# Kernel tuning notes

Hardware: AMD Instinct MI355X
Metric: run time of the kernel (lower is better)

The kernel has to match this reference:

```python
import jax, jax.numpy as jnp
import numpy as np

DIM = 256


def setup_inputs() -> dict:
    key = jax.random.key(0)
    ks = jax.random.split(key, 10)
    d = DIM
    inp = {
        "agent": jax.random.normal(ks[0], (64, d), dtype=jnp.float32),
        "x": jax.random.normal(ks[1], (8, 4096, d), dtype=jnp.float32),
        # parameters (stored as [in, out]; y = x @ W + b)
        "W_qkv": jax.random.normal(ks[2], (d, 3 * d), dtype=jnp.float32) * (d ** -0.5),
        "b_qkv": jnp.zeros((3 * d,), dtype=jnp.float32),
        "W_agent": jax.random.normal(ks[3], (d, 2 * d), dtype=jnp.float32) * (d ** -0.5),
        "b_agent": jnp.zeros((2 * d,), dtype=jnp.float32),
        "W_fc1": jax.random.normal(ks[4], (d, d), dtype=jnp.float32) * (d ** -0.5),
        "b_fc1": jnp.zeros((d,), dtype=jnp.float32),
        "W_fc2": jax.random.normal(ks[5], (d, d), dtype=jnp.float32) * (d ** -0.5),
        "b_fc2": jnp.zeros((d,), dtype=jnp.float32),
    }
    return inp


def reference(agent, x, W_qkv, b_qkv, W_agent, b_agent, W_fc1, b_fc1, W_fc2, b_fc2):
    d = x.shape[-1]
    scale = d ** -0.5
    # qkv projection of tokens: [B,N,3d] -> q,k,v each [B,N,d]
    qkv = x @ W_qkv + b_qkv
    q, k, v = jnp.split(qkv, 3, axis=-1)
    # agent projection: [K,2d] -> q_agent,k_agent each [K,d]
    ag = agent @ W_agent + b_agent
    q_agent, k_agent = jnp.split(ag, 2, axis=-1)
    # stage 1: agents attend over tokens -> [B,K,N]
    attn1 = jax.nn.softmax(jnp.einsum('kd,bnd->bkn', q_agent, k) * scale, axis=-1)
    va = jnp.einsum('bkn,bnd->bkd', attn1, v)  # [B,K,d]
    va = va @ W_fc1 + b_fc1
    # stage 2: tokens attend over agents -> [B,N,K]
    attn2 = jax.nn.softmax(jnp.einsum('bnd,kd->bnk', q, k_agent) * scale, axis=-1)
    out = jnp.einsum('bnk,bkd->bnd', attn2, va)  # [B,N,d]
    out = out @ W_fc2 + b_fc2
    return out + x
```

## Files before the change

### kernel.cpp

```cpp
#include <hip/hip_runtime.h>
#include <stdint.h>
#include <string.h>

#define BB 8
#define NN 4096
#define DD 256
#define SCALE 0.0625f
#define XS2 264

using frag_ab = __attribute__((ext_vector_type(8))) short;
using frag_cd = __attribute__((ext_vector_type(4))) float;

__device__ __forceinline__ unsigned short f2bf(float f) {
    union { float f; unsigned u; } a; a.f = f;
    unsigned r = a.u + 0x7FFFu + ((a.u >> 16) & 1u);
    return (unsigned short)(r >> 16);
}
__device__ __forceinline__ float bf2f(unsigned short h) {
    union { unsigned u; float f; } a; a.u = ((unsigned)h) << 16;
    return a.f;
}

__global__ __launch_bounds__(256) void k_setup(
    const float* __restrict__ agent, const float* __restrict__ Wag,
    const float* __restrict__ bag, const float* __restrict__ Wqkv,
    const float* __restrict__ bqkv, const float* __restrict__ Wfc1,
    const float* __restrict__ bfc1, const float* __restrict__ Wfc2,
    unsigned short* __restrict__ P12t, float* __restrict__ c2,
    unsigned short* __restrict__ W3b, float* __restrict__ b3)
{
    __shared__ float arow[256];
    __shared__ float red[256];
    const int bx = blockIdx.x, tid = threadIdx.x;
    if (bx < 128) {
        const int c = bx;
        const int woff = (c < 64) ? 256 : 0;
        const int aoff = (c < 64) ? 0 : 256;
        const int row = c & 63;
        float s = bag[aoff + tid];
        for (int o = 0; o < 256; ++o) s += agent[row * 256 + o] * Wag[o * 512 + aoff + tid];
        arow[tid] = s;
        __syncthreads();
        float p = 0.f;
        for (int o = 0; o < 256; ++o) p += Wqkv[tid * 768 + woff + o] * arow[o];
        P12t[(size_t)c * 256 + tid] = f2bf(SCALE * p);
        if (c >= 64) {
            red[tid] = bqkv[woff + tid] * arow[tid];
            __syncthreads();
            for (int st = 128; st; st >>= 1) {
                if (tid < st) red[tid] += red[tid + st];
                __syncthreads();
            }
            if (tid == 0) c2[c - 64] = SCALE * red[0];
        }
    } else if (bx < 384) {
        const int i = bx - 128;
        float t = 0.f;
        for (int o = 0; o < 256; ++o) t += Wqkv[i * 768 + 512 + o] * Wfc1[o * 256 + tid];
        arow[tid] = t;
        __syncthreads();
        float p = 0.f;
        for (int k = 0; k < 256; ++k) p += arow[k] * Wfc2[k * 256 + tid];
        W3b[(size_t)i * 256 + tid] = f2bf(p);
    } else {
        float t = bfc1[tid];
        for (int o = 0; o < 256; ++o) t += bqkv[512 + o] * Wfc1[o * 256 + tid];
        arow[tid] = t;
        __syncthreads();
        float p = 0.f;
        for (int k = 0; k < 256; ++k) p += arow[k] * Wfc2[k * 256 + tid];
        b3[tid] = p;
    }
}

__global__ __launch_bounds__(256) void k_xlogits(
    const float* __restrict__ x, const unsigned short* __restrict__ P12t,
    const float* __restrict__ c2, unsigned short* __restrict__ xt,
    unsigned short* __restrict__ p1, unsigned short* __restrict__ p2b,
    float* __restrict__ statS)
{
    __shared__ unsigned short xtile[32 * XS2];
    __shared__ unsigned short Bs[128 * 72];
    __shared__ float Ss[2][64];
    const int chunk = blockIdx.x, b = blockIdx.y;
    const int n0 = chunk * 32;
    const int tid = threadIdx.x;
    const int w = tid >> 6, lane = tid & 63;
    const int ml = lane & 15, q = lane >> 4;
    const int rt = w & 1, cg = w >> 1;

#pragma unroll
    for (int p = 0; p < 8; ++p) {
        int idx = p * 256 + tid;
        int tok = idx >> 6, d = (idx & 63) * 4;
        float4 v = *(const float4*)&x[(size_t)(b * 4096 + n0 + tok) * 256 + d];
        unsigned short u[4] = {f2bf(v.x), f2bf(v.y), f2bf(v.z), f2bf(v.w)};
        uint2 pk; memcpy(&pk, u, 8);
        *(uint2*)&xtile[tok * XS2 + d] = pk;
    }
    __syncthreads();
#pragma unroll
    for (int p = 0; p < 8; ++p) {
        int idx = p * 256 + tid;
        int d = idx >> 3, seg = idx & 7;
        unsigned short u[4];
#pragma unroll
        for (int k = 0; k < 4; ++k) u[k] = xtile[(seg * 4 + k) * XS2 + d];
        uint2 pk; memcpy(&pk, u, 8);
        *(uint2*)&xt[(size_t)(b * 256 + d) * 4096 + n0 + seg * 4] = pk;
    }

    frag_cd acc[4];
#pragma unroll
    for (int j = 0; j < 4; ++j)
#pragma unroll
        for (int r = 0; r < 4; ++r) acc[j][r] = 0.f;

    for (int kb = 0; kb < 256; kb += 64) {
        __syncthreads();
#pragma unroll
        for (int p = 0; p < 4; ++p) {
            int idx = p * 256 + tid;
            int r = idx >> 3, c = (idx & 7) * 8;
            *(uint4*)&Bs[r * 72 + c] = *(const uint4*)&P12t[(size_t)r * 256 + kb + c];
        }
        __syncthreads();
#pragma unroll
        for (int ks = 0; ks < 2; ++ks) {
            const int kk = ks * 32 + q * 8;
            frag_ab a = *(const frag_ab*)&xtile[(rt * 16 + ml) * XS2 + kb + kk];
#pragma unroll
            for (int j = 0; j < 4; ++j) {
                frag_ab bf = *(const frag_ab*)&Bs[(cg * 64 + j * 16 + ml) * 72 + kk];
                acc[j] = __builtin_amdgcn_mfma_f32_16x16x32_bf16(a, bf, acc[j], 0, 0, 0);
            }
        }
    }

    if (cg == 0) {
#pragma unroll
        for (int j = 0; j < 4; ++j) {
            const int ag = j * 16 + ml;
            float e[4];
#pragma unroll
            for (int r = 0; r < 4; ++r) e[r] = __expf(acc[j][r]);
            unsigned short u[4] = {f2bf(e[0]), f2bf(e[1]), f2bf(e[2]), f2bf(e[3])};
            uint2 pk; memcpy(&pk, u, 8);
            *(uint2*)&p1[(size_t)(b * 64 + ag) * 4096 + n0 + rt * 16 + q * 4] = pk;
            float s = e[0] + e[1] + e[2] + e[3];
            s += __shfl_xor(s, 16);
            s += __shfl_xor(s, 32);
            if (q == 0) Ss[rt][ag] = s;
        }
    } else {
        float cc[4];
#pragma unroll
        for (int j = 0; j < 4; ++j) cc[j] = c2[j * 16 + ml];
#pragma unroll
        for (int r = 0; r < 4; ++r) {
            float e[4], s = 0.f;
#pragma unroll
            for (int j = 0; j < 4; ++j) {
                e[j] = __expf(acc[j][r] + cc[j]);
                s += e[j];
            }
#pragma unroll
            for (int mask = 1; mask <= 8; mask <<= 1) s += __shfl_xor(s, mask);
            float inv = 1.f / s;
            const int tok = n0 + rt * 16 + q * 4 + r;
#pragma unroll
            for (int j = 0; j < 4; ++j)
                p2b[(size_t)(b * 4096 + tok) * 64 + j * 16 + ml] = f2bf(e[j] * inv);
        }
    }
    __syncthreads();
    if (tid < 64)
        statS[(size_t)(b * 64 + tid) * 128 + chunk] = Ss[0][tid] + Ss[1][tid];
}

__global__ __launch_bounds__(256) void k_va(
    const unsigned short* __restrict__ p1, const float* __restrict__ statS,
    const unsigned short* __restrict__ xt, unsigned short* __restrict__ part)
{
    __shared__ unsigned short As[64 * 152];
    __shared__ unsigned short Bs[64 * 152];
    __shared__ float Rs[4][64], Inv[64];
    const int s = blockIdx.x, dh = blockIdx.y, b = blockIdx.z;
    const int tid = threadIdx.x;
    const int w = tid >> 6, lane = tid & 63;
    const int ml = lane & 15, q = lane >> 4;

#pragma unroll
    for (int p = 0; p < 4; ++p) {
        int idx = p * 256 + tid;
        int r = idx >> 4, c = (idx & 15) * 8;
        *(uint4*)&Bs[r * 152 + c] =
            *(const uint4*)&xt[(size_t)(b * 256 + dh * 64 + r) * 4096 + s * 128 + c];
    }
    {
        const int a = tid & 63, qq = tid >> 6;
        const float* ps = &statS[(size_t)(b * 64 + a) * 128 + qq * 32];
        float sum = 0.f;
#pragma unroll
        for (int p = 0; p < 8; ++p) {
            float4 s4 = *(const float4*)&ps[p * 4];
            sum += s4.x + s4.y + s4.z + s4.w;
        }
        Rs[qq][a] = sum;
    }
    __syncthreads();
    if (tid < 64)
        Inv[tid] = 1.f / (Rs[0][tid] + Rs[1][tid] + Rs[2][tid] + Rs[3][tid]);
    __syncthreads();
#pragma unroll
    for (int p = 0; p < 8; ++p) {
        int idx4 = (p * 256 + tid) * 4;
        int ag = idx4 >> 7, t = idx4 & 127;
        uint2 pk = *(const uint2*)&p1[(size_t)(b * 64 + ag) * 4096 + s * 128 + t];
        unsigned short in[4]; memcpy(in, &pk, 8);
        float inv = Inv[ag];
        unsigned short u[4] = {f2bf(bf2f(in[0]) * inv), f2bf(bf2f(in[1]) * inv),
                               f2bf(bf2f(in[2]) * inv), f2bf(bf2f(in[3]) * inv)};
        uint2 po; memcpy(&po, u, 8);
        *(uint2*)&As[ag * 152 + t] = po;
    }
    __syncthreads();

    frag_cd acc[4];
#pragma unroll
    for (int i = 0; i < 4; ++i)
#pragma unroll
        for (int r = 0; r < 4; ++r) acc[i][r] = 0.f;
#pragma unroll
    for (int ks = 0; ks < 4; ++ks) {
        const int kk = ks * 32 + q * 8;
        frag_ab bf = *(const frag_ab*)&Bs[(w * 16 + ml) * 152 + kk];
#pragma unroll
        for (int i = 0; i < 4; ++i) {
            frag_ab a = *(const frag_ab*)&As[(i * 16 + ml) * 152 + kk];
            acc[i] = __builtin_amdgcn_mfma_f32_16x16x32_bf16(a, bf, acc[i], 0, 0, 0);
        }
    }
    const int d = dh * 64 + w * 16 + ml;
#pragma unroll
    for (int i = 0; i < 4; ++i)
#pragma unroll
        for (int r = 0; r < 4; ++r)
            part[(size_t)((s * 8 + b) * 64 + i * 16 + q * 4 + r) * 256 + d] =
                f2bf(acc[i][r]);
}

__global__ __launch_bounds__(256) void k_fc(
    const unsigned short* __restrict__ part, const unsigned short* __restrict__ W3b,
    const float* __restrict__ b3, unsigned short* __restrict__ va3t)
{
    __shared__ float rowb[256];
    const int row = blockIdx.x, tid = threadIdx.x;
    const int b = row >> 6, agc = row & 63;
    float sv = 0.f;
    for (int s = 0; s < 32; ++s)
        sv += bf2f(part[(size_t)((s * 8 + b) * 64 + agc) * 256 + tid]);
    rowb[tid] = sv;
    __syncthreads();
    float s2 = b3[tid];
    for (int k = 0; k < 256; ++k) s2 += rowb[k] * bf2f(W3b[(size_t)k * 256 + tid]);
    va3t[(size_t)(b * 256 + tid) * 64 + agc] = f2bf(s2);
}

__global__ __launch_bounds__(256) void k_stage2(
    const unsigned short* __restrict__ p2b, const unsigned short* __restrict__ va3t,
    const float* __restrict__ x, const float* __restrict__ bfc2,
    float* __restrict__ out)
{
    __shared__ unsigned short Vs[256 * 72];
    __shared__ unsigned short Ps[64 * 72];
    const int n0 = blockIdx.x * 64, b = blockIdx.y;
    const int tid = threadIdx.x;
    const int w = tid >> 6, lane = tid & 63;
    const int ml = lane & 15, q = lane >> 4;

#pragma unroll
    for (int p = 0; p < 8; ++p) {
        int idx = p * 256 + tid;
        int r = idx >> 3, c = (idx & 7) * 8;
        *(uint4*)&Vs[r * 72 + c] = *(const uint4*)&va3t[(size_t)(b * 256 + r) * 64 + c];
    }
#pragma unroll
    for (int p = 0; p < 2; ++p) {
        int idx = p * 256 + tid;
        int r = idx >> 3, c = (idx & 7) * 8;
        *(uint4*)&Ps[r * 72 + c] = *(const uint4*)&p2b[(size_t)(b * 4096 + n0 + r) * 64 + c];
    }
    __syncthreads();

    frag_cd acc[4][4];
#pragma unroll
    for (int i = 0; i < 4; ++i)
#pragma unroll
        for (int j = 0; j < 4; ++j)
#pragma unroll
            for (int r = 0; r < 4; ++r) acc[i][j][r] = 0.f;
#pragma unroll
    for (int ks = 0; ks < 2; ++ks) {
        const int kk = ks * 32 + q * 8;
        frag_ab a[4], bf[4];
#pragma unroll
        for (int i = 0; i < 4; ++i)
            a[i] = *(const frag_ab*)&Vs[(w * 64 + i * 16 + ml) * 72 + kk];
#pragma unroll
        for (int j = 0; j < 4; ++j)
            bf[j] = *(const frag_ab*)&Ps[(j * 16 + ml) * 72 + kk];
#pragma unroll
        for (int i = 0; i < 4; ++i)
#pragma unroll
            for (int j = 0; j < 4; ++j)
                acc[i][j] = __builtin_amdgcn_mfma_f32_16x16x32_bf16(
                    a[i], bf[j], acc[i][j], 0, 0, 0);
    }

#pragma unroll
    for (int i = 0; i < 4; ++i) {
        const int d0 = w * 64 + i * 16 + q * 4;
        float4 bias = *(const float4*)&bfc2[d0];
#pragma unroll
        for (int j = 0; j < 4; ++j) {
            const int tok = n0 + j * 16 + ml;
            size_t ad = (size_t)(b * 4096 + tok) * 256 + d0;
            float4 xr = *(const float4*)&x[ad];
            float4 o;
            o.x = acc[i][j][0] + bias.x + xr.x;
            o.y = acc[i][j][1] + bias.y + xr.y;
            o.z = acc[i][j][2] + bias.z + xr.z;
            o.w = acc[i][j][3] + bias.w + xr.w;
            *(float4*)&out[ad] = o;
        }
    }
}

extern "C" void kernel_launch(void* const* d_in, const int* in_sizes, int n_in,
                              void* d_out, int out_size, void* d_ws, size_t ws_size,
                              hipStream_t stream) {
    const float* agent = (const float*)d_in[0];
    const float* x     = (const float*)d_in[1];
    const float* Wqkv  = (const float*)d_in[2];
    const float* bqkv  = (const float*)d_in[3];
    const float* Wag   = (const float*)d_in[4];
    const float* bag   = (const float*)d_in[5];
    const float* Wfc1  = (const float*)d_in[6];
    const float* bfc1  = (const float*)d_in[7];
    const float* Wfc2  = (const float*)d_in[8];
    const float* bfc2  = (const float*)d_in[9];
    float* out = (float*)d_out;

    char* w = (char*)d_ws;
    size_t off = 0;
    unsigned short* xt   = (unsigned short*)(w + off); off += (size_t)BB * DD * NN * 2;
    unsigned short* p1   = (unsigned short*)(w + off); off += (size_t)BB * 64 * NN * 2;
    unsigned short* p2b  = (unsigned short*)(w + off); off += (size_t)BB * NN * 64 * 2;
    unsigned short* part = (unsigned short*)(w + off); off += (size_t)32 * BB * 64 * 256 * 2;
    float* statS = (float*)(w + off); off += (size_t)BB * 64 * 128 * 4;
    unsigned short* P12t = (unsigned short*)(w + off); off += (size_t)128 * 256 * 2;
    float* c2   = (float*)(w + off); off += 256 * 4;
    unsigned short* W3b = (unsigned short*)(w + off); off += (size_t)256 * 256 * 2;
    float* b3   = (float*)(w + off); off += 256 * 4;
    unsigned short* va3t = (unsigned short*)(w + off); off += (size_t)BB * DD * 64 * 2;

    k_setup<<<385, 256, 0, stream>>>(agent, Wag, bag, Wqkv, bqkv, Wfc1, bfc1, Wfc2,
                                     P12t, c2, W3b, b3);
    k_xlogits<<<dim3(128, BB), 256, 0, stream>>>(x, P12t, c2, xt, p1, p2b, statS);
    k_va<<<dim3(32, 4, BB), 256, 0, stream>>>(p1, statS, xt, part);
    k_fc<<<512, 256, 0, stream>>>(part, W3b, b3, va3t);
    k_stage2<<<dim3(64, BB), 256, 0, stream>>>(p2b, va3t, x, bfc2, out);
}
```

Baseline: 169.7 us.

## Fuse logits and value-aggregation kernels, keeping x tile in shared memory

Merges the logits kernel and the agent-value aggregation kernel into one kernel per 64-token chunk. The bf16 x tile stays in LDS and is reused as the B operand for the P1·x MFMA, so the transposed x copy and the unnormalized p1 matrix no longer go through global memory. Softmax normalization for stage 1 moves into k_fc, which now sums per-chunk statistics and divides after reducing partials. In exchange there are twice as many partial slabs to reduce in k_fc, more registers per thread, strided LDS reads when building the x fragments, and only 512 blocks for the fused kernel.

```diff
diff --git a/kernel.cpp b/kernel.cpp
--- a/kernel.cpp
+++ b/kernel.cpp
@@ -6,7 +6,8 @@
 #define NN 4096
 #define DD 256
 #define SCALE 0.0625f
-#define XS2 264
+#define XS 264
+#define XT 72
 
 using frag_ab = __attribute__((ext_vector_type(8))) short;
 using frag_cd = __attribute__((ext_vector_type(4))) float;
@@ -73,48 +74,37 @@
     }
 }
 
-__global__ __launch_bounds__(256) void k_xlogits(
+__global__ __launch_bounds__(256) void k_fuse(
     const float* __restrict__ x, const unsigned short* __restrict__ P12t,
-    const float* __restrict__ c2, unsigned short* __restrict__ xt,
-    unsigned short* __restrict__ p1, unsigned short* __restrict__ p2b,
-    float* __restrict__ statS)
+    const float* __restrict__ c2, unsigned short* __restrict__ p2b,
+    unsigned short* __restrict__ part, float* __restrict__ statS)
 {
-    __shared__ unsigned short xtile[32 * XS2];
-    __shared__ unsigned short Bs[128 * 72];
-    __shared__ float Ss[2][64];
-    const int chunk = blockIdx.x, b = blockIdx.y;
-    const int n0 = chunk * 32;
+    __shared__ unsigned short xtile[64 * XS];
+    __shared__ unsigned short Bs[128 * XT];
+    __shared__ unsigned short Pl[64 * XT];
+    __shared__ float Ss[4][64];
+    const int s = blockIdx.x, b = blockIdx.y;
+    const int n0 = s * 64;
     const int tid = threadIdx.x;
     const int w = tid >> 6, lane = tid & 63;
     const int ml = lane & 15, q = lane >> 4;
-    const int rt = w & 1, cg = w >> 1;
-
-#pragma unroll
-    for (int p = 0; p < 8; ++p) {
+
+#pragma unroll
+    for (int p = 0; p < 16; ++p) {
         int idx = p * 256 + tid;
         int tok = idx >> 6, d = (idx & 63) * 4;
         float4 v = *(const float4*)&x[(size_t)(b * 4096 + n0 + tok) * 256 + d];
         unsigned short u[4] = {f2bf(v.x), f2bf(v.y), f2bf(v.z), f2bf(v.w)};
         uint2 pk; memcpy(&pk, u, 8);
-        *(uint2*)&xtile[tok * XS2 + d] = pk;
-    }
-    __syncthreads();
-#pragma unroll
-    for (int p = 0; p < 8; ++p) {
-        int idx = p * 256 + tid;
-        int d = idx >> 3, seg = idx & 7;
-        unsigned short u[4];
-#pragma unroll
-        for (int k = 0; k < 4; ++k) u[k] = xtile[(seg * 4 + k) * XS2 + d];
-        uint2 pk; memcpy(&pk, u, 8);
-        *(uint2*)&xt[(size_t)(b * 256 + d) * 4096 + n0 + seg * 4] = pk;
-    }
-
-    frag_cd acc[4];
-#pragma unroll
-    for (int j = 0; j < 4; ++j)
-#pragma unroll
-        for (int r = 0; r < 4; ++r) acc[j][r] = 0.f;
+        *(uint2*)&xtile[tok * XS + d] = pk;
+    }
+    __syncthreads();
+
+    frag_cd acc1[8];
+#pragma unroll
+    for (int j = 0; j < 8; ++j)
+#pragma unroll
+        for (int r = 0; r < 4; ++r) acc1[j][r] = 0.f;
 
     for (int kb = 0; kb < 256; kb += 64) {
         __syncthreads();
@@ -122,145 +112,122 @@
         for (int p = 0; p < 4; ++p) {
             int idx = p * 256 + tid;
             int r = idx >> 3, c = (idx & 7) * 8;
-            *(uint4*)&Bs[r * 72 + c] = *(const uint4*)&P12t[(size_t)r * 256 + kb + c];
+            *(uint4*)&Bs[r * XT + c] = *(const uint4*)&P12t[(size_t)r * 256 + kb + c];
         }
         __syncthreads();
 #pragma unroll
         for (int ks = 0; ks < 2; ++ks) {
             const int kk = ks * 32 + q * 8;
-            frag_ab a = *(const frag_ab*)&xtile[(rt * 16 + ml) * XS2 + kb + kk];
+            frag_ab a = *(const frag_ab*)&xtile[(w * 16 + ml) * XS + kb + kk];
+#pragma unroll
+            for (int j = 0; j < 8; ++j) {
+                frag_ab bf = *(const frag_ab*)&Bs[(j * 16 + ml) * XT + kk];
+                acc1[j] = __builtin_amdgcn_mfma_f32_16x16x32_bf16(a, bf, acc1[j], 0, 0, 0);
+            }
+        }
+    }
+
+    {
+        float cc[4];
+#pragma unroll
+        for (int j = 0; j < 4; ++j) cc[j] = c2[j * 16 + ml];
+#pragma unroll
+        for (int r = 0; r < 4; ++r) {
+            float e[4], sum = 0.f;
 #pragma unroll
             for (int j = 0; j < 4; ++j) {
-                frag_ab bf = *(const frag_ab*)&Bs[(cg * 64 + j * 16 + ml) * 72 + kk];
-                acc[j] = __builtin_amdgcn_mfma_f32_16x16x32_bf16(a, bf, acc[j], 0, 0, 0);
+                e[j] = __expf(acc1[4 + j][r] + cc[j]);
+                sum += e[j];
             }
-        }
-    }
-
-    if (cg == 0) {
-#pragma unroll
-        for (int j = 0; j < 4; ++j) {
-            const int ag = j * 16 + ml;
-            float e[4];
-#pragma unroll
-            for (int r = 0; r < 4; ++r) e[r] = __expf(acc[j][r]);
-            unsigned short u[4] = {f2bf(e[0]), f2bf(e[1]), f2bf(e[2]), f2bf(e[3])};
-            uint2 pk; memcpy(&pk, u, 8);
-            *(uint2*)&p1[(size_t)(b * 64 + ag) * 4096 + n0 + rt * 16 + q * 4] = pk;
-            float s = e[0] + e[1] + e[2] + e[3];
-            s += __shfl_xor(s, 16);
-            s += __shfl_xor(s, 32);
-            if (q == 0) Ss[rt][ag] = s;
-        }
-    } else {
-        float cc[4];
-#pragma unroll
-        for (int j = 0; j < 4; ++j) cc[j] = c2[j * 16 + ml];
-#pragma unroll
-        for (int r = 0; r < 4; ++r) {
-            float e[4], s = 0.f;
-#pragma unroll
-            for (int j = 0; j < 4; ++j) {
-                e[j] = __expf(acc[j][r] + cc[j]);
-                s += e[j];
-            }
-#pragma unroll
-            for (int mask = 1; mask <= 8; mask <<= 1) s += __shfl_xor(s, mask);
-            float inv = 1.f / s;
-            const int tok = n0 + rt * 16 + q * 4 + r;
+#pragma unroll
+            for (int mask = 1; mask <= 8; mask <<= 1) sum += __shfl_xor(sum, mask);
+            float inv = 1.f / sum;
+            const int tok = n0 + w * 16 + q * 4 + r;
 #pragma unroll
             for (int j = 0; j < 4; ++j)
                 p2b[(size_t)(b * 4096 + tok) * 64 + j * 16 + ml] = f2bf(e[j] * inv);
         }
     }
-    __syncthreads();
+
+    float e1[4][4];
+#pragma unroll
+    for (int j = 0; j < 4; ++j) {
+#pragma unroll
+        for (int r = 0; r < 4; ++r) e1[j][r] = __expf(acc1[j][r]);
+        float sj = e1[j][0] + e1[j][1] + e1[j][2] + e1[j][3];
+        sj += __shfl_xor(sj, 16);
+        sj += __shfl_xor(sj, 32);
+        if (lane < 16) Ss[w][j * 16 + ml] = sj;
+    }
+
+#pragma unroll
+    for (int j = 0; j < 4; ++j)
+#pragma unroll
+        for (int r = 0; r < 4; ++r)
+            Pl[(j * 16 + ml) * XT + w * 16 + q * 4 + r] = f2bf(e1[j][r]);
+    __syncthreads();
+
     if (tid < 64)
-        statS[(size_t)(b * 64 + tid) * 128 + chunk] = Ss[0][tid] + Ss[1][tid];
-}
-
-__global__ __launch_bounds__(256) void k_va(
-    const unsigned short* __restrict__ p1, const float* __restrict__ statS,
-    const unsigned short* __restrict__ xt, unsigned short* __restrict__ part)
-{
-    __shared__ unsigned short As[64 * 152];
-    __shared__ unsigned short Bs[64 * 152];
-    __shared__ float Rs[4][64], Inv[64];
-    const int s = blockIdx.x, dh = blockIdx.y, b = blockIdx.z;
-    const int tid = threadIdx.x;
-    const int w = tid >> 6, lane = tid & 63;
-    const int ml = lane & 15, q = lane >> 4;
-
-#pragma unroll
-    for (int p = 0; p < 4; ++p) {
-        int idx = p * 256 + tid;
-        int r = idx >> 4, c = (idx & 15) * 8;
-        *(uint4*)&Bs[r * 152 + c] =
-            *(const uint4*)&xt[(size_t)(b * 256 + dh * 64 + r) * 4096 + s * 128 + c];
-    }
-    {
-        const int a = tid & 63, qq = tid >> 6;
-        const float* ps = &statS[(size_t)(b * 64 + a) * 128 + qq * 32];
-        float sum = 0.f;
-#pragma unroll
-        for (int p = 0; p < 8; ++p) {
-            float4 s4 = *(const float4*)&ps[p * 4];
-            sum += s4.x + s4.y + s4.z + s4.w;
-        }
-        Rs[qq][a] = sum;
-    }
-    __syncthreads();
-    if (tid < 64)
-        Inv[tid] = 1.f / (Rs[0][tid] + Rs[1][tid] + Rs[2][tid] + Rs[3][tid]);
-    __syncthreads();
-#pragma unroll
-    for (int p = 0; p < 8; ++p) {
-        int idx4 = (p * 256 + tid) * 4;
-        int ag = idx4 >> 7, t = idx4 & 127;
-        uint2 pk = *(const uint2*)&p1[(size_t)(b * 64 + ag) * 4096 + s * 128 + t];
-        unsigned short in[4]; memcpy(in, &pk, 8);
-        float inv = Inv[ag];
-        unsigned short u[4] = {f2bf(bf2f(in[0]) * inv), f2bf(bf2f(in[1]) * inv),
-                               f2bf(bf2f(in[2]) * inv), f2bf(bf2f(in[3]) * inv)};
-        uint2 po; memcpy(&po, u, 8);
-        *(uint2*)&As[ag * 152 + t] = po;
-    }
-    __syncthreads();
-
-    frag_cd acc[4];
-#pragma unroll
-    for (int i = 0; i < 4; ++i)
-#pragma unroll
-        for (int r = 0; r < 4; ++r) acc[i][r] = 0.f;
-#pragma unroll
-    for (int ks = 0; ks < 4; ++ks) {
+        statS[(size_t)(b * 64 + tid) * 64 + s] =
+            Ss[0][tid] + Ss[1][tid] + Ss[2][tid] + Ss[3][tid];
+
+    frag_cd acc2[4][4];
+#pragma unroll
+    for (int af = 0; af < 4; ++af)
+#pragma unroll
+        for (int i = 0; i < 4; ++i)
+#pragma unroll
+            for (int r = 0; r < 4; ++r) acc2[af][i][r] = 0.f;
+#pragma unroll
+    for (int ks = 0; ks < 2; ++ks) {
         const int kk = ks * 32 + q * 8;
-        frag_ab bf = *(const frag_ab*)&Bs[(w * 16 + ml) * 152 + kk];
+        frag_ab a[4], bf[4];
+#pragma unroll
+        for (int af = 0; af < 4; ++af)
+            a[af] = *(const frag_ab*)&Pl[(af * 16 + ml) * XT + kk];
 #pragma unroll
         for (int i = 0; i < 4; ++i) {
-            frag_ab a = *(const frag_ab*)&As[(i * 16 + ml) * 152 + kk];
-            acc[i] = __builtin_amdgcn_mfma_f32_16x16x32_bf16(a, bf, acc[i], 0, 0, 0);
-        }
-    }
-    const int d = dh * 64 + w * 16 + ml;
-#pragma unroll
-    for (int i = 0; i < 4; ++i)
-#pragma unroll
-        for (int r = 0; r < 4; ++r)
-            part[(size_t)((s * 8 + b) * 64 + i * 16 + q * 4 + r) * 256 + d] =
-                f2bf(acc[i][r]);
+            const int d = w * 64 + i * 16 + ml;
+            unsigned short u[8];
+#pragma unroll
+            for (int t = 0; t < 8; ++t) u[t] = xtile[(kk + t) * XS + d];
+            memcpy(&bf[i], u, 16);
+        }
+#pragma unroll
+        for (int af = 0; af < 4; ++af)
+#pragma unroll
+            for (int i = 0; i < 4; ++i)
+                acc2[af][i] = __builtin_amdgcn_mfma_f32_16x16x32_bf16(
+                    a[af], bf[i], acc2[af][i], 0, 0, 0);
+    }
+#pragma unroll
+    for (int af = 0; af < 4; ++af)
+#pragma unroll
+        for (int i = 0; i < 4; ++i)
+#pragma unroll
+            for (int r = 0; r < 4; ++r)
+                part[(size_t)((s * 8 + b) * 64 + af * 16 + q * 4 + r) * 256 +
+                     w * 64 + i * 16 + ml] = f2bf(acc2[af][i][r]);
 }
 
 __global__ __launch_bounds__(256) void k_fc(
-    const unsigned short* __restrict__ part, const unsigned short* __restrict__ W3b,
-    const float* __restrict__ b3, unsigned short* __restrict__ va3t)
+    const unsigned short* __restrict__ part, const float* __restrict__ statS,
+    const unsigned short* __restrict__ W3b, const float* __restrict__ b3,
+    unsigned short* __restrict__ va3t)
 {
     __shared__ float rowb[256];
+    __shared__ float rs[64];
     const int row = blockIdx.x, tid = threadIdx.x;
     const int b = row >> 6, agc = row & 63;
+    if (tid < 64) rs[tid] = statS[(size_t)(b * 64 + agc) * 64 + tid];
     float sv = 0.f;
-    for (int s = 0; s < 32; ++s)
+    for (int s = 0; s < 64; ++s)
         sv += bf2f(part[(size_t)((s * 8 + b) * 64 + agc) * 256 + tid]);
-    rowb[tid] = sv;
+    __syncthreads();
+    float tot = 0.f;
+#pragma unroll
+    for (int t = 0; t < 64; ++t) tot += rs[t];
+    rowb[tid] = sv / tot;
     __syncthreads();
     float s2 = b3[tid];
     for (int k = 0; k < 256; ++k) s2 += rowb[k] * bf2f(W3b[(size_t)k * 256 + tid]);
@@ -354,11 +321,9 @@
 
     char* w = (char*)d_ws;
     size_t off = 0;
-    unsigned short* xt   = (unsigned short*)(w + off); off += (size_t)BB * DD * NN * 2;
-    unsigned short* p1   = (unsigned short*)(w + off); off += (size_t)BB * 64 * NN * 2;
     unsigned short* p2b  = (unsigned short*)(w + off); off += (size_t)BB * NN * 64 * 2;
-    unsigned short* part = (unsigned short*)(w + off); off += (size_t)32 * BB * 64 * 256 * 2;
-    float* statS = (float*)(w + off); off += (size_t)BB * 64 * 128 * 4;
+    unsigned short* part = (unsigned short*)(w + off); off += (size_t)64 * BB * 64 * 256 * 2;
+    float* statS = (float*)(w + off); off += (size_t)BB * 64 * 64 * 4;
     unsigned short* P12t = (unsigned short*)(w + off); off += (size_t)128 * 256 * 2;
     float* c2   = (float*)(w + off); off += 256 * 4;
     unsigned short* W3b = (unsigned short*)(w + off); off += (size_t)256 * 256 * 2;
@@ -367,8 +332,7 @@
 
     k_setup<<<385, 256, 0, stream>>>(agent, Wag, bag, Wqkv, bqkv, Wfc1, bfc1, Wfc2,
                                      P12t, c2, W3b, b3);
-    k_xlogits<<<dim3(128, BB), 256, 0, stream>>>(x, P12t, c2, xt, p1, p2b, statS);
-    k_va<<<dim3(32, 4, BB), 256, 0, stream>>>(p1, statS, xt, part);
-    k_fc<<<512, 256, 0, stream>>>(part, W3b, b3, va3t);
+    k_fuse<<<dim3(64, BB), 256, 0, stream>>>(x, P12t, c2, p2b, part, statS);
+    k_fc<<<512, 256, 0, stream>>>(part, statS, W3b, b3, va3t);
     k_stage2<<<dim3(64, BB), 256, 0, stream>>>(p2b, va3t, x, bfc2, out);
 }
```

New measurement: 160.9 us. 1.05x faster.
